# Kernel optimization log

Hardware: AMD Instinct MI355X
Metric: run time of the kernel (lower is better)

The kernel has to match this reference:

```python
import jax, jax.numpy as jnp
import numpy as np

B, H, L, D, LBL = 512, 64, 528, 32, 10
NI = 64          # number of interval breakpoints
W = 128          # vf MLP width
N_STEPS = 256    # fixed Tsit5 steps over [t0, t1]

# Tsit5 Butcher tableau
C2, C3, C4, C5, C6 = 0.161, 0.327, 0.9, 0.9800255409045097, 1.0
A21 = 0.161
A31, A32 = -0.008480655492356989, 0.335480655492357
A41, A42, A43 = 2.8971530571054935, -6.359448489975075, 4.3622954328695815
A51, A52, A53, A54 = 5.325864828439257, -11.748883564062828, 7.4955393428898365, -0.09249506636175525
A61, A62, A63, A64, A65 = 5.86145544294642, -12.92096931784711, 8.159367898576159, -0.071584973281401, -0.028269050394068383
B1, B2, B3, B4, B5, B6 = 0.09646076681806523, 0.01, 0.4798896504144996, 1.379008574103742, -3.290069515436081, 2.324710524099774


def _linear_init(k, out_dim, in_dim):
    lim = 1.0 / np.sqrt(in_dim)
    kw, kb = jax.random.split(k)
    w = jax.random.uniform(kw, (out_dim, in_dim), jnp.float32, -lim, lim)
    b = jax.random.uniform(kb, (out_dim,), jnp.float32, -lim, lim)
    return w, b


def setup_inputs() -> dict:
    key = jax.random.key(0)
    ks = jax.random.split(key, 8)
    ts = jnp.linspace(0.0, 1.0, 129, dtype=jnp.float32)
    logsig = 0.1 * jax.random.normal(ks[0], (B, NI + 1, L + 1), jnp.float32)
    x0 = jax.random.normal(ks[1], (B, D), jnp.float32)
    intervals = jnp.linspace(0.0, 1.0, NI, dtype=jnp.float32)
    vf_w0, vf_b0 = _linear_init(ks[2], W, H)
    vf_w1, vf_b1 = _linear_init(ks[3], W, W)
    vf_w2, vf_b2 = _linear_init(ks[4], W, W)
    vf_w3, vf_b3 = _linear_init(ks[5], H * L, W)
    l1_w, l1_b = _linear_init(ks[6], H, D)
    l2_w, l2_b = _linear_init(ks[7], LBL, H)
    return dict(ts=ts, logsig=logsig, x0=x0, intervals=intervals,
                vf_w0=vf_w0, vf_b0=vf_b0, vf_w1=vf_w1, vf_b1=vf_b1,
                vf_w2=vf_w2, vf_b2=vf_b2, vf_w3=vf_w3, vf_b3=vf_b3,
                l1_w=l1_w, l1_b=l1_b, l2_w=l2_w, l2_b=l2_b)


def reference(ts, logsig, x0, intervals,
              vf_w0, vf_b0, vf_w1, vf_b1, vf_w2, vf_b2, vf_w3, vf_b3,
              l1_w, l1_b, l2_w, l2_b):
    Bn = x0.shape[0]
    Hn = l1_w.shape[0]
    Ln = vf_b3.shape[0] // Hn

    def vf(y):  # y: (B, H) -> (B, H, L)
        h = jax.nn.silu(y @ vf_w0.T + vf_b0)
        h = jax.nn.silu(h @ vf_w1.T + vf_b1)
        h = jax.nn.silu(h @ vf_w2.T + vf_b2)
        out = jnp.tanh(h @ vf_w3.T + vf_b3)
        return out.reshape(Bn, Hn, Ln)

    def func(t, y):
        idx = jnp.searchsorted(intervals, t)
        sig = logsig[:, idx, 1:]          # (B, L)
        return jnp.einsum('bhl,bl->bh', vf(y), sig)

    t0, t1 = ts[0], ts[-1]
    dt = (t1 - t0) / N_STEPS

    def step(y, i):
        t = t0 + i * dt
        k1 = func(t, y)
        k2 = func(t + C2 * dt, y + dt * (A21 * k1))
        k3 = func(t + C3 * dt, y + dt * (A31 * k1 + A32 * k2))
        k4 = func(t + C4 * dt, y + dt * (A41 * k1 + A42 * k2 + A43 * k3))
        k5 = func(t + C5 * dt, y + dt * (A51 * k1 + A52 * k2 + A53 * k3 + A54 * k4))
        k6 = func(t + C6 * dt, y + dt * (A61 * k1 + A62 * k2 + A63 * k3 + A64 * k4 + A65 * k5))
        y_new = y + dt * (B1 * k1 + B2 * k2 + B3 * k3 + B4 * k4 + B5 * k5 + B6 * k6)
        return y_new, None

    y0 = x0 @ l1_w.T + l1_b
    yT, _ = jax.lax.scan(step, y0, jnp.arange(N_STEPS, dtype=jnp.float32))
    return jax.nn.softmax(yT @ l2_w.T + l2_b, axis=-1)
```

## Files before the change

kernel.cpp:

```cpp
#include <hip/hip_runtime.h>
#include <stdint.h>

#define NBLK 256
#define NTHR 512

typedef __attribute__((ext_vector_type(8))) short short8;
typedef __attribute__((ext_vector_type(4))) float float4_;

#define WS_BAR  0
#define WS_HDNF 16384
#define WS_KF   (16384 + 131072)

#define LOADC(p)    __hip_atomic_load((p),  __ATOMIC_RELAXED, __HIP_MEMORY_SCOPE_SYSTEM)
#define STOREC(p,v) __hip_atomic_store((p), (v), __ATOMIC_RELAXED, __HIP_MEMORY_SCOPE_SYSTEM)

__device__ __forceinline__ unsigned short f2bf(float x) {
  union { float f; unsigned u; } v; v.f = x;
  return (unsigned short)((v.u + 0x7fffu + ((v.u >> 16) & 1u)) >> 16);
}
__device__ __forceinline__ float fast_exp(float x) {
  return __builtin_amdgcn_exp2f(x * 1.4426950408889634f);
}
__device__ __forceinline__ float fast_tanh(float x) {
  float e = __builtin_amdgcn_exp2f(x * 2.8853900817779268f);
  return fmaf(-2.0f, __builtin_amdgcn_rcpf(e + 1.0f), 1.0f);
}
__device__ __forceinline__ float fast_silu(float x) {
  float e = fast_exp(-x);
  return x * __builtin_amdgcn_rcpf(1.0f + e);
}

__device__ __forceinline__ void rgbar(unsigned* bar, int h, int Rg, unsigned bn) {
  __syncthreads();
  if (threadIdx.x == 0) {
    unsigned* base = bar + 32 * (32 + Rg * 16);
    unsigned* leaf = base + 32 * (h & 7);
    unsigned* root = base + 32 * 8;
    unsigned* gen  = base + 32 * 9;
    unsigned a = __hip_atomic_fetch_add(leaf, 1u, __ATOMIC_RELAXED, __HIP_MEMORY_SCOPE_SYSTEM);
    if (a == 8u * bn - 1u) {
      unsigned r = __hip_atomic_fetch_add(root, 1u, __ATOMIC_RELAXED, __HIP_MEMORY_SCOPE_SYSTEM);
      if (r == 8u * bn - 1u) STOREC(gen, bn);
    }
    while (LOADC(gen) < bn) __builtin_amdgcn_s_sleep(1);
  }
  __syncthreads();
}

template<int SIN>
__device__ __forceinline__ void rk_stage(
    int stepi, int sg, int h, int Rg, int R, int r0,
    float (&kh)[6], float& y, float t0v, float dtv,
    const float4_ (&wr1)[16], const float4_ (&wr2)[16],
    float b0r, float b1r, float b2r,
    unsigned char* ws, unsigned* BAR, unsigned& rseq,
    const float* logsig, const float* w0,
    unsigned short* w3lds, float* b3lds, float* intv,
    float (*yst)[64], float (*hb1)[128], float (*hb2)[128],
    unsigned short (*hdnS)[128], int* sidxp) {
  const int tid = threadIdx.x;
  const int lane = tid & 63, wv = tid >> 6;
  const int col = lane & 15, qd = lane >> 4;
  const int mrow = tid >> 8, mj = ((tid >> 6) & 3) * 32 + (tid & 31), mhalf = (tid >> 5) & 1;
  unsigned* HDNF = (unsigned*)(ws + WS_HDNF);
  float* KF  = (float*)(ws + WS_KF);

  if (sg > 0 && tid < 128) {
    const float* KFr = KF + ((sg & 1) ^ 1) * 32768;
    constexpr int pi = (SIN == 0) ? 5 : SIN - 1;
    kh[pi] = LOADC(&KFr[(size_t)(r0 + (tid >> 6)) * 64 + (tid & 63)]);
  }
  if (tid < 128) {
    float ystv;
    if constexpr (SIN == 0) {
      if (sg > 0) {
        y += dtv * (0.09646076681806523f * kh[0] + 0.01f * kh[1]
                  + 0.4798896504144996f * kh[2] + 1.379008574103742f * kh[3]
                  - 3.290069515436081f * kh[4] + 2.324710524099774f * kh[5]);
      }
      ystv = y;
    } else if constexpr (SIN == 1) {
      ystv = y + dtv * (0.161f * kh[0]);
    } else if constexpr (SIN == 2) {
      ystv = y + dtv * (-0.008480655492356989f * kh[0] + 0.335480655492357f * kh[1]);
    } else if constexpr (SIN == 3) {
      ystv = y + dtv * (2.8971530571054935f * kh[0] - 6.359448489975075f * kh[1]
                      + 4.3622954328695815f * kh[2]);
    } else if constexpr (SIN == 4) {
      ystv = y + dtv * (5.325864828439257f * kh[0] - 11.748883564062828f * kh[1]
                      + 7.4955393428898365f * kh[2] - 0.09249506636175525f * kh[3]);
    } else {
      ystv = y + dtv * (5.86145544294642f * kh[0] - 12.92096931784711f * kh[1]
                      + 8.159367898576159f * kh[2] - 0.071584973281401f * kh[3]
                      - 0.028269050394068383f * kh[4]);
    }
    yst[tid >> 6][tid & 63] = ystv;
  }
  {
    float tb = __fadd_rn(t0v, __fmul_rn((float)stepi, dtv));
    float t_cur;
    if constexpr (SIN == 0) t_cur = tb;
    else {
      constexpr float cS = (SIN == 1) ? 0.161f : (SIN == 2) ? 0.327f : (SIN == 3) ? 0.9f
                         : (SIN == 4) ? 0.9800255409045097f : 1.0f;
      t_cur = __fadd_rn(tb, __fmul_rn(cS, dtv));
    }
    if (tid < 64) {
      unsigned long long m1 = __ballot(intv[tid] < t_cur);
      if (tid == 0) *sidxp = (int)__popcll(m1);
    }
  }
  __syncthreads();
  const int idx = *sidxp;

  {
    const float4_* wrp = (const float4_*)(w0 + (size_t)mj * 64 + mhalf * 32);
    const float* yp = &yst[mrow][mhalf * 32];
    float ac0 = 0.0f, ac1 = 0.0f;
    #pragma unroll
    for (int i4 = 0; i4 < 8; ++i4) {
      float4_ wvv = wrp[i4];
      float s = fmaf(yp[4*i4+0], wvv[0], yp[4*i4+1] * wvv[1]);
      s = fmaf(yp[4*i4+2], wvv[2], s);
      s = fmaf(yp[4*i4+3], wvv[3], s);
      if (i4 & 1) ac1 += s; else ac0 += s;
    }
    float v = ac0 + ac1;
    v += __shfl_xor(v, 32);
    if (mhalf == 0) hb1[mrow][mj] = fast_silu(v + b0r);
  }
  __syncthreads();
  {
    const float* hp = &hb1[mrow][mhalf * 64];
    float ac0 = 0.0f, ac1 = 0.0f;
    #pragma unroll
    for (int i4 = 0; i4 < 16; ++i4) {
      float4_ wvv = wr1[i4];
      float s = fmaf(hp[4*i4+0], wvv[0], hp[4*i4+1] * wvv[1]);
      s = fmaf(hp[4*i4+2], wvv[2], s);
      s = fmaf(hp[4*i4+3], wvv[3], s);
      if (i4 & 1) ac1 += s; else ac0 += s;
    }
    float v = ac0 + ac1;
    v += __shfl_xor(v, 32);
    if (mhalf == 0) hb2[mrow][mj] = fast_silu(v + b1r);
  }
  __syncthreads();
  {
    const float* hp = &hb2[mrow][mhalf * 64];
    float ac0 = 0.0f, ac1 = 0.0f;
    #pragma unroll
    for (int i4 = 0; i4 < 16; ++i4) {
      float4_ wvv = wr2[i4];
      float s = fmaf(hp[4*i4+0], wvv[0], hp[4*i4+1] * wvv[1]);
      s = fmaf(hp[4*i4+2], wvv[2], s);
      s = fmaf(hp[4*i4+3], wvv[3], s);
      if (i4 & 1) ac1 += s; else ac0 += s;
    }
    float v = ac0 + ac1;
    v += __shfl_xor(v, 32);
    if (mhalf == 0) hdnS[mrow][mj] = f2bf(fast_silu(v + b2r));
  }
  __syncthreads();
  if (tid < 128) {
    const int row = tid >> 6, u = tid & 63;
    const int lb = 2 * h + row;
    const int tile = lb >> 4, colp = lb & 15;
    const int j0 = 2 * u;
    const int kb = j0 >> 5, qdp = (j0 >> 3) & 3, jj = j0 & 7;
    unsigned v = (unsigned)hdnS[row][j0] | ((unsigned)hdnS[row][j0 + 1] << 16);
    unsigned i16 = (unsigned)((Rg * 32 + tile * 4 + kb) * 512 + qdp * 128 + colp * 8 + jj);
    STOREC(&HDNF[i16 >> 1], v);
  }
  ++rseq; rgbar(BAR, h, Rg, rseq);

  {
    const unsigned long long* H64 = (const unsigned long long*)HDNF;
    union { unsigned long long u[2]; short8 s; } af[4];
    #pragma unroll
    for (int kb = 0; kb < 4; ++kb) {
      const unsigned i16 = (unsigned)((Rg * 32 + wv * 4 + kb) * 512 + lane * 8);
      af[kb].u[0] = LOADC(&H64[i16 >> 2]);
      af[kb].u[1] = LOADC(&H64[(i16 >> 2) + 1]);
    }
    const float* sp0 = logsig + (size_t)(R + wv * 16 + qd * 4) * 34385 + (size_t)idx * 529 + 1;
    const float* sp1 = sp0 + 34385;
    const float* sp2 = sp0 + 2 * 34385;
    const float* sp3 = sp0 + 3 * 34385;
    float kp[4] = {0.0f, 0.0f, 0.0f, 0.0f};
    #pragma unroll 2
    for (int nt = 0; nt < 33; ++nt) {
      const int l = nt * 16 + col;
      const float bv = b3lds[l];
      float4_ acc; acc[0] = bv; acc[1] = bv; acc[2] = bv; acc[3] = bv;
      #pragma unroll
      for (int kb = 0; kb < 4; ++kb) {
        const short8 bf = *(const short8*)(w3lds + ((nt * 4 + kb) * 64 + lane) * 8);
        acc = __builtin_amdgcn_mfma_f32_16x16x32_bf16(af[kb].s, bf, acc, 0, 0, 0);
      }
      kp[0] = fmaf(fast_tanh(acc[0]), sp0[l], kp[0]);
      kp[1] = fmaf(fast_tanh(acc[1]), sp1[l], kp[1]);
      kp[2] = fmaf(fast_tanh(acc[2]), sp2[l], kp[2]);
      kp[3] = fmaf(fast_tanh(acc[3]), sp3[l], kp[3]);
    }
    #pragma unroll
    for (int r = 0; r < 4; ++r) {
      float v = kp[r];
      v += __shfl_xor(v, 1); v += __shfl_xor(v, 2);
      v += __shfl_xor(v, 4); v += __shfl_xor(v, 8);
      kp[r] = v;
    }
    if (col == 0) {
      float* KFw = KF + (sg & 1) * 32768;
      #pragma unroll
      for (int r = 0; r < 4; ++r)
        STOREC(&KFw[(size_t)(R + wv * 16 + qd * 4 + r) * 64 + h], kp[r]);
    }
  }
  ++rseq; rgbar(BAR, h, Rg, rseq);
}

__global__ void __launch_bounds__(NTHR, 2)
rde_kernel(const float* __restrict__ ts, const float* __restrict__ logsig,
           const float* __restrict__ x0, const float* __restrict__ intervals,
           const float* __restrict__ w0, const float* __restrict__ b0,
           const float* __restrict__ w1, const float* __restrict__ b1,
           const float* __restrict__ w2, const float* __restrict__ b2,
           const float* __restrict__ w3, const float* __restrict__ b3,
           const float* __restrict__ l1w, const float* __restrict__ l1b,
           const float* __restrict__ l2w, const float* __restrict__ l2b,
           float* out, unsigned char* ws) {
  const int tid = threadIdx.x;
  const int g = blockIdx.x;
  const int Rg = (g >> 1) & 3;
  const int h  = ((g >> 3) << 1) | (g & 1);
  const int R = Rg * 128;
  const int r0 = R + 2 * h;
  unsigned* BAR = (unsigned*)(ws + WS_BAR);
  unsigned rseq = 0;

  __shared__ __attribute__((aligned(16))) unsigned short w3lds[67584];
  __shared__ float b3lds[528];
  __shared__ float intv[64];
  __shared__ float yst[2][64];
  __shared__ float hb1[2][128];
  __shared__ float hb2[2][128];
  __shared__ __attribute__((aligned(8))) unsigned short hdnS[2][128];
  __shared__ int sidx;

  if (tid < 64) intv[tid] = intervals[tid];
  for (int e = tid; e < 528; e += NTHR) b3lds[e] = b3[(size_t)h * 528 + e];

  for (int e = tid; e < 8448; e += NTHR) {
    const int ln = e & 63, kb = (e >> 6) & 3, nt = e >> 8;
    const float* src = w3 + ((size_t)(h * 528 + nt * 16 + (ln & 15))) * 128 + kb * 32 + (ln >> 4) * 8;
    union { unsigned short s[8]; short8 v; } p;
    #pragma unroll
    for (int j = 0; j < 8; ++j) p.s[j] = f2bf(src[j]);
    *(short8*)(w3lds + e * 8) = p.v;
  }

  const int mj = ((tid >> 6) & 3) * 32 + (tid & 31), mhalf = (tid >> 5) & 1;
  float4_ wr1[16], wr2[16];
  {
    const float4_* s1 = (const float4_*)(w1 + (size_t)mj * 128 + mhalf * 64);
    const float4_* s2 = (const float4_*)(w2 + (size_t)mj * 128 + mhalf * 64);
    #pragma unroll
    for (int i = 0; i < 16; ++i) { wr1[i] = s1[i]; wr2[i] = s2[i]; }
  }
  const float b0r = b0[mj], b1r = b1[mj], b2r = b2[mj];

  float y = 0.0f, kh[6];
  #pragma unroll
  for (int i = 0; i < 6; ++i) kh[i] = 0.0f;
  if (tid < 128) {
    const int row = tid >> 6, hh = tid & 63;
    float acc = l1b[hh];
    const float4_* xr = (const float4_*)(x0 + (size_t)(r0 + row) * 32);
    const float4_* wr = (const float4_*)(l1w + (size_t)hh * 32);
    #pragma unroll
    for (int d = 0; d < 8; ++d) {
      float4_ xv = xr[d], wvv = wr[d];
      acc = fmaf(xv[0], wvv[0], acc); acc = fmaf(xv[1], wvv[1], acc);
      acc = fmaf(xv[2], wvv[2], acc); acc = fmaf(xv[3], wvv[3], acc);
    }
    y = acc;
  }
  const float t0v = ts[0];
  const float dtv = (ts[128] - t0v) * (1.0f / 256.0f);
  __syncthreads();

  for (int stepi = 0; stepi < 256; ++stepi) {
    const int sg = stepi * 6;
    rk_stage<0>(stepi, sg + 0, h, Rg, R, r0, kh, y, t0v, dtv, wr1, wr2, b0r, b1r, b2r,
                ws, BAR, rseq, logsig, w0, w3lds, b3lds, intv, yst, hb1, hb2, hdnS, &sidx);
    rk_stage<1>(stepi, sg + 1, h, Rg, R, r0, kh, y, t0v, dtv, wr1, wr2, b0r, b1r, b2r,
                ws, BAR, rseq, logsig, w0, w3lds, b3lds, intv, yst, hb1, hb2, hdnS, &sidx);
    rk_stage<2>(stepi, sg + 2, h, Rg, R, r0, kh, y, t0v, dtv, wr1, wr2, b0r, b1r, b2r,
                ws, BAR, rseq, logsig, w0, w3lds, b3lds, intv, yst, hb1, hb2, hdnS, &sidx);
    rk_stage<3>(stepi, sg + 3, h, Rg, R, r0, kh, y, t0v, dtv, wr1, wr2, b0r, b1r, b2r,
                ws, BAR, rseq, logsig, w0, w3lds, b3lds, intv, yst, hb1, hb2, hdnS, &sidx);
    rk_stage<4>(stepi, sg + 4, h, Rg, R, r0, kh, y, t0v, dtv, wr1, wr2, b0r, b1r, b2r,
                ws, BAR, rseq, logsig, w0, w3lds, b3lds, intv, yst, hb1, hb2, hdnS, &sidx);
    rk_stage<5>(stepi, sg + 5, h, Rg, R, r0, kh, y, t0v, dtv, wr1, wr2, b0r, b1r, b2r,
                ws, BAR, rseq, logsig, w0, w3lds, b3lds, intv, yst, hb1, hb2, hdnS, &sidx);
  }

  {
    float* KF = (float*)(ws + WS_KF);
    if (tid < 128) {
      const int row = tid >> 6, hh = tid & 63;
      kh[5] = LOADC(&KF[(size_t)32768 + (size_t)(r0 + row) * 64 + hh]);
      y += dtv * (0.09646076681806523f * kh[0] + 0.01f * kh[1]
                + 0.4798896504144996f * kh[2] + 1.379008574103742f * kh[3]
                - 3.290069515436081f * kh[4] + 2.324710524099774f * kh[5]);
      yst[row][hh] = y;
    }
    __syncthreads();
    if (tid < 20) {
      const int row = tid / 10, c = tid % 10;
      float acc = l2b[c];
      const float* wr = l2w + c * 64;
      #pragma unroll
      for (int i2 = 0; i2 < 64; ++i2) acc = fmaf(yst[row][i2], wr[i2], acc);
      hb1[row][c] = acc;
    }
    __syncthreads();
    if (tid < 2) {
      const int row = tid;
      float mx = -1e30f;
      for (int c = 0; c < 10; ++c) mx = fmaxf(mx, hb1[row][c]);
      float ev[10], den = 0.0f;
      for (int c = 0; c < 10; ++c) { ev[c] = expf(hb1[row][c] - mx); den += ev[c]; }
      const float rd = 1.0f / den;
      for (int c = 0; c < 10; ++c) out[(size_t)(r0 + row) * 10 + c] = ev[c] * rd;
    }
  }
}

extern "C" void kernel_launch(void* const* d_in, const int* in_sizes, int n_in,
                              void* d_out, int out_size, void* d_ws, size_t ws_size,
                              hipStream_t stream) {
  (void)in_sizes; (void)n_in; (void)out_size; (void)ws_size;
  const float* ts        = (const float*)d_in[0];
  const float* logsig    = (const float*)d_in[1];
  const float* x0        = (const float*)d_in[2];
  const float* intervals = (const float*)d_in[3];
  const float* w0        = (const float*)d_in[4];
  const float* b0        = (const float*)d_in[5];
  const float* w1        = (const float*)d_in[6];
  const float* b1        = (const float*)d_in[7];
  const float* w2        = (const float*)d_in[8];
  const float* b2        = (const float*)d_in[9];
  const float* w3        = (const float*)d_in[10];
  const float* b3        = (const float*)d_in[11];
  const float* l1w       = (const float*)d_in[12];
  const float* l1b       = (const float*)d_in[13];
  const float* l2w       = (const float*)d_in[14];
  const float* l2b       = (const float*)d_in[15];
  float* out = (float*)d_out;
  unsigned char* ws = (unsigned char*)d_ws;

  hipMemsetAsync(d_ws, 0, 12288, stream);

  void* args[] = { &ts, &logsig, &x0, &intervals, &w0, &b0, &w1, &b1,
                   &w2, &b2, &w3, &b3, &l1w, &l1b, &l2w, &l2b, &out, &ws };
  hipLaunchCooperativeKernel((void*)rde_kernel, dim3(NBLK), dim3(NTHR), args, 0, stream);
}
```

Before: 42.98 ms.

## Compute hidden MLP redundantly per block with MFMA, removing one grid barrier per stage

Each block now computes the three hidden MLP layers for all 128 rows of its group with bf16 MFMA, using weights pre-packed into the workspace. The y state is published through global memory instead of the hidden activations, so each RK stage needs one group barrier instead of two. The RK state update also moves into the MFMA output layout. The cost is redundant hidden-layer compute in every block, bf16 precision in the hidden layers (y is split into hi/lo bf16 parts for the first layer), and launch bounds lowered to one block per SIMD set.

```diff
diff --git a/kernel.cpp b/kernel.cpp
--- a/kernel.cpp
+++ b/kernel.cpp
@@ -8,8 +8,10 @@
 typedef __attribute__((ext_vector_type(4))) float float4_;
 
 #define WS_BAR  0
-#define WS_HDNF 16384
-#define WS_KF   (16384 + 131072)
+#define WS_YST  16384
+#define WS_W0F  (16384 + 262144)
+#define WS_W1F  (WS_W0F + 16384)
+#define WS_W2F  (WS_W1F + 32768)
 
 #define LOADC(p)    __hip_atomic_load((p),  __ATOMIC_RELAXED, __HIP_MEMORY_SCOPE_SYSTEM)
 #define STOREC(p,v) __hip_atomic_store((p), (v), __ATOMIC_RELAXED, __HIP_MEMORY_SCOPE_SYSTEM)
@@ -17,6 +19,9 @@
 __device__ __forceinline__ unsigned short f2bf(float x) {
   union { float f; unsigned u; } v; v.f = x;
   return (unsigned short)((v.u + 0x7fffu + ((v.u >> 16) & 1u)) >> 16);
+}
+__device__ __forceinline__ float bf2f(unsigned short s) {
+  union { unsigned u; float f; } v; v.u = ((unsigned)s) << 16; return v.f;
 }
 __device__ __forceinline__ float fast_exp(float x) {
   return __builtin_amdgcn_exp2f(x * 1.4426950408889634f);
@@ -47,55 +52,60 @@
   __syncthreads();
 }
 
+template<int SINN>
+__device__ __forceinline__ void rk_publish(float (&yv)[4], const float (&khv)[6][4],
+                                           float dtv, int col, int mrow0, int h,
+                                           float* YW) {
+  float ystv[4];
+  #pragma unroll
+  for (int r = 0; r < 4; ++r) {
+    if constexpr (SINN == 0) {
+      yv[r] += dtv * (0.09646076681806523f * khv[0][r] + 0.01f * khv[1][r]
+                    + 0.4798896504144996f * khv[2][r] + 1.379008574103742f * khv[3][r]
+                    - 3.290069515436081f * khv[4][r] + 2.324710524099774f * khv[5][r]);
+      ystv[r] = yv[r];
+    } else if constexpr (SINN == 1) {
+      ystv[r] = yv[r] + dtv * (0.161f * khv[0][r]);
+    } else if constexpr (SINN == 2) {
+      ystv[r] = yv[r] + dtv * (-0.008480655492356989f * khv[0][r]
+                             + 0.335480655492357f * khv[1][r]);
+    } else if constexpr (SINN == 3) {
+      ystv[r] = yv[r] + dtv * (2.8971530571054935f * khv[0][r]
+                             - 6.359448489975075f * khv[1][r]
+                             + 4.3622954328695815f * khv[2][r]);
+    } else if constexpr (SINN == 4) {
+      ystv[r] = yv[r] + dtv * (5.325864828439257f * khv[0][r]
+                             - 11.748883564062828f * khv[1][r]
+                             + 7.4955393428898365f * khv[2][r]
+                             - 0.09249506636175525f * khv[3][r]);
+    } else {
+      ystv[r] = yv[r] + dtv * (5.86145544294642f * khv[0][r]
+                             - 12.92096931784711f * khv[1][r]
+                             + 8.159367898576159f * khv[2][r]
+                             - 0.071584973281401f * khv[3][r]
+                             - 0.028269050394068383f * khv[4][r]);
+    }
+  }
+  if (col == 0) {
+    #pragma unroll
+    for (int r = 0; r < 4; ++r)
+      STOREC(&YW[(size_t)(mrow0 + r) * 64 + h], ystv[r]);
+  }
+}
+
 template<int SIN>
 __device__ __forceinline__ void rk_stage(
-    int stepi, int sg, int h, int Rg, int R, int r0,
-    float (&kh)[6], float& y, float t0v, float dtv,
-    const float4_ (&wr1)[16], const float4_ (&wr2)[16],
-    float b0r, float b1r, float b2r,
+    int stepi, int sg, int h, int Rg, int R,
+    float (&yv)[4], float (&khv)[6][4], float t0v, float dtv,
     unsigned char* ws, unsigned* BAR, unsigned& rseq,
-    const float* logsig, const float* w0,
+    const float* logsig, const float* b0, const float* b1, const float* b2,
     unsigned short* w3lds, float* b3lds, float* intv,
-    float (*yst)[64], float (*hb1)[128], float (*hb2)[128],
-    unsigned short (*hdnS)[128], int* sidxp) {
+    unsigned short* bounce, int* sidxp) {
   const int tid = threadIdx.x;
   const int lane = tid & 63, wv = tid >> 6;
   const int col = lane & 15, qd = lane >> 4;
-  const int mrow = tid >> 8, mj = ((tid >> 6) & 3) * 32 + (tid & 31), mhalf = (tid >> 5) & 1;
-  unsigned* HDNF = (unsigned*)(ws + WS_HDNF);
-  float* KF  = (float*)(ws + WS_KF);
-
-  if (sg > 0 && tid < 128) {
-    const float* KFr = KF + ((sg & 1) ^ 1) * 32768;
-    constexpr int pi = (SIN == 0) ? 5 : SIN - 1;
-    kh[pi] = LOADC(&KFr[(size_t)(r0 + (tid >> 6)) * 64 + (tid & 63)]);
-  }
-  if (tid < 128) {
-    float ystv;
-    if constexpr (SIN == 0) {
-      if (sg > 0) {
-        y += dtv * (0.09646076681806523f * kh[0] + 0.01f * kh[1]
-                  + 0.4798896504144996f * kh[2] + 1.379008574103742f * kh[3]
-                  - 3.290069515436081f * kh[4] + 2.324710524099774f * kh[5]);
-      }
-      ystv = y;
-    } else if constexpr (SIN == 1) {
-      ystv = y + dtv * (0.161f * kh[0]);
-    } else if constexpr (SIN == 2) {
-      ystv = y + dtv * (-0.008480655492356989f * kh[0] + 0.335480655492357f * kh[1]);
-    } else if constexpr (SIN == 3) {
-      ystv = y + dtv * (2.8971530571054935f * kh[0] - 6.359448489975075f * kh[1]
-                      + 4.3622954328695815f * kh[2]);
-    } else if constexpr (SIN == 4) {
-      ystv = y + dtv * (5.325864828439257f * kh[0] - 11.748883564062828f * kh[1]
-                      + 7.4955393428898365f * kh[2] - 0.09249506636175525f * kh[3]);
-    } else {
-      ystv = y + dtv * (5.86145544294642f * kh[0] - 12.92096931784711f * kh[1]
-                      + 8.159367898576159f * kh[2] - 0.071584973281401f * kh[3]
-                      - 0.028269050394068383f * kh[4]);
-    }
-    yst[tid >> 6][tid & 63] = ystv;
-  }
+  const int mrow0 = R + wv * 16 + qd * 4;
+
   {
     float tb = __fadd_rn(t0v, __fmul_rn((float)stepi, dtv));
     float t_cur;
@@ -113,81 +123,99 @@
   __syncthreads();
   const int idx = *sidxp;
 
-  {
-    const float4_* wrp = (const float4_*)(w0 + (size_t)mj * 64 + mhalf * 32);
-    const float* yp = &yst[mrow][mhalf * 32];
-    float ac0 = 0.0f, ac1 = 0.0f;
-    #pragma unroll
-    for (int i4 = 0; i4 < 8; ++i4) {
-      float4_ wvv = wrp[i4];
-      float s = fmaf(yp[4*i4+0], wvv[0], yp[4*i4+1] * wvv[1]);
-      s = fmaf(yp[4*i4+2], wvv[2], s);
-      s = fmaf(yp[4*i4+3], wvv[3], s);
-      if (i4 & 1) ac1 += s; else ac0 += s;
-    }
-    float v = ac0 + ac1;
-    v += __shfl_xor(v, 32);
-    if (mhalf == 0) hb1[mrow][mj] = fast_silu(v + b0r);
-  }
-  __syncthreads();
-  {
-    const float* hp = &hb1[mrow][mhalf * 64];
-    float ac0 = 0.0f, ac1 = 0.0f;
-    #pragma unroll
-    for (int i4 = 0; i4 < 16; ++i4) {
-      float4_ wvv = wr1[i4];
-      float s = fmaf(hp[4*i4+0], wvv[0], hp[4*i4+1] * wvv[1]);
-      s = fmaf(hp[4*i4+2], wvv[2], s);
-      s = fmaf(hp[4*i4+3], wvv[3], s);
-      if (i4 & 1) ac1 += s; else ac0 += s;
-    }
-    float v = ac0 + ac1;
-    v += __shfl_xor(v, 32);
-    if (mhalf == 0) hb2[mrow][mj] = fast_silu(v + b1r);
-  }
-  __syncthreads();
-  {
-    const float* hp = &hb2[mrow][mhalf * 64];
-    float ac0 = 0.0f, ac1 = 0.0f;
-    #pragma unroll
-    for (int i4 = 0; i4 < 16; ++i4) {
-      float4_ wvv = wr2[i4];
-      float s = fmaf(hp[4*i4+0], wvv[0], hp[4*i4+1] * wvv[1]);
-      s = fmaf(hp[4*i4+2], wvv[2], s);
-      s = fmaf(hp[4*i4+3], wvv[3], s);
-      if (i4 & 1) ac1 += s; else ac0 += s;
-    }
-    float v = ac0 + ac1;
-    v += __shfl_xor(v, 32);
-    if (mhalf == 0) hdnS[mrow][mj] = f2bf(fast_silu(v + b2r));
-  }
-  __syncthreads();
-  if (tid < 128) {
-    const int row = tid >> 6, u = tid & 63;
-    const int lb = 2 * h + row;
-    const int tile = lb >> 4, colp = lb & 15;
-    const int j0 = 2 * u;
-    const int kb = j0 >> 5, qdp = (j0 >> 3) & 3, jj = j0 & 7;
-    unsigned v = (unsigned)hdnS[row][j0] | ((unsigned)hdnS[row][j0 + 1] << 16);
-    unsigned i16 = (unsigned)((Rg * 32 + tile * 4 + kb) * 512 + qdp * 128 + colp * 8 + jj);
-    STOREC(&HDNF[i16 >> 1], v);
-  }
-  ++rseq; rgbar(BAR, h, Rg, rseq);
-
-  {
-    const unsigned long long* H64 = (const unsigned long long*)HDNF;
-    union { unsigned long long u[2]; short8 s; } af[4];
-    #pragma unroll
-    for (int kb = 0; kb < 4; ++kb) {
-      const unsigned i16 = (unsigned)((Rg * 32 + wv * 4 + kb) * 512 + lane * 8);
-      af[kb].u[0] = LOADC(&H64[i16 >> 2]);
-      af[kb].u[1] = LOADC(&H64[(i16 >> 2) + 1]);
-    }
-    const float* sp0 = logsig + (size_t)(R + wv * 16 + qd * 4) * 34385 + (size_t)idx * 529 + 1;
+  short8 af[4];
+  {
+    const float* YR = (const float*)(ws + WS_YST) + (size_t)(sg & 1) * 32768;
+    const short8* W0F = (const short8*)(ws + WS_W0F);
+    const short8* W1F = (const short8*)(ws + WS_W1F);
+    const short8* W2F = (const short8*)(ws + WS_W2F);
+    unsigned short* M = bounce + wv * 512;
+
+    short8 a1hi[2], a1lo[2];
+    #pragma unroll
+    for (int kb = 0; kb < 2; ++kb) {
+      union { unsigned long long u[4]; float f[8]; } yr;
+      const unsigned long long* ya = (const unsigned long long*)
+          (YR + (size_t)(R + wv * 16 + (lane & 15)) * 64 + kb * 32 + qd * 8);
+      #pragma unroll
+      for (int j = 0; j < 4; ++j) yr.u[j] = LOADC(ya + j);
+      union { unsigned short s[8]; short8 v; } hi, lo;
+      #pragma unroll
+      for (int j = 0; j < 8; ++j) {
+        unsigned short hb = f2bf(yr.f[j]);
+        hi.s[j] = hb;
+        lo.s[j] = f2bf(yr.f[j] - bf2f(hb));
+      }
+      a1hi[kb] = hi.v; a1lo[kb] = lo.v;
+    }
+
+    short8 a2[4];
+    #pragma unroll
+    for (int kp2 = 0; kp2 < 4; ++kp2) {
+      #pragma unroll
+      for (int th = 0; th < 2; ++th) {
+        const int t = kp2 * 2 + th;
+        float4_ c; c[0] = 0.0f; c[1] = 0.0f; c[2] = 0.0f; c[3] = 0.0f;
+        #pragma unroll
+        for (int kb = 0; kb < 2; ++kb) {
+          const short8 bf = W0F[(t * 2 + kb) * 64 + lane];
+          c = __builtin_amdgcn_mfma_f32_16x16x32_bf16(a1hi[kb], bf, c, 0, 0, 0);
+          c = __builtin_amdgcn_mfma_f32_16x16x32_bf16(a1lo[kb], bf, c, 0, 0, 0);
+        }
+        const float bv = b0[t * 16 + col];
+        #pragma unroll
+        for (int r = 0; r < 4; ++r)
+          M[(qd * 4 + r) * 32 + th * 16 + col] = f2bf(fast_silu(c[r] + bv));
+      }
+      a2[kp2] = *(const short8*)&M[(lane & 15) * 32 + qd * 8];
+    }
+
+    short8 a3[4];
+    #pragma unroll
+    for (int kp2 = 0; kp2 < 4; ++kp2) {
+      #pragma unroll
+      for (int th = 0; th < 2; ++th) {
+        const int t = kp2 * 2 + th;
+        float4_ c; c[0] = 0.0f; c[1] = 0.0f; c[2] = 0.0f; c[3] = 0.0f;
+        #pragma unroll
+        for (int kb = 0; kb < 4; ++kb) {
+          const short8 bf = W1F[(t * 4 + kb) * 64 + lane];
+          c = __builtin_amdgcn_mfma_f32_16x16x32_bf16(a2[kb], bf, c, 0, 0, 0);
+        }
+        const float bv = b1[t * 16 + col];
+        #pragma unroll
+        for (int r = 0; r < 4; ++r)
+          M[(qd * 4 + r) * 32 + th * 16 + col] = f2bf(fast_silu(c[r] + bv));
+      }
+      a3[kp2] = *(const short8*)&M[(lane & 15) * 32 + qd * 8];
+    }
+
+    #pragma unroll
+    for (int kp2 = 0; kp2 < 4; ++kp2) {
+      #pragma unroll
+      for (int th = 0; th < 2; ++th) {
+        const int t = kp2 * 2 + th;
+        float4_ c; c[0] = 0.0f; c[1] = 0.0f; c[2] = 0.0f; c[3] = 0.0f;
+        #pragma unroll
+        for (int kb = 0; kb < 4; ++kb) {
+          const short8 bf = W2F[(t * 4 + kb) * 64 + lane];
+          c = __builtin_amdgcn_mfma_f32_16x16x32_bf16(a3[kb], bf, c, 0, 0, 0);
+        }
+        const float bv = b2[t * 16 + col];
+        #pragma unroll
+        for (int r = 0; r < 4; ++r)
+          M[(qd * 4 + r) * 32 + th * 16 + col] = f2bf(fast_silu(c[r] + bv));
+      }
+      af[kp2] = *(const short8*)&M[(lane & 15) * 32 + qd * 8];
+    }
+  }
+
+  float kp[4] = {0.0f, 0.0f, 0.0f, 0.0f};
+  {
+    const float* sp0 = logsig + (size_t)mrow0 * 34385 + (size_t)idx * 529 + 1;
     const float* sp1 = sp0 + 34385;
     const float* sp2 = sp0 + 2 * 34385;
     const float* sp3 = sp0 + 3 * 34385;
-    float kp[4] = {0.0f, 0.0f, 0.0f, 0.0f};
     #pragma unroll 2
     for (int nt = 0; nt < 33; ++nt) {
       const int l = nt * 16 + col;
@@ -196,7 +224,7 @@
       #pragma unroll
       for (int kb = 0; kb < 4; ++kb) {
         const short8 bf = *(const short8*)(w3lds + ((nt * 4 + kb) * 64 + lane) * 8);
-        acc = __builtin_amdgcn_mfma_f32_16x16x32_bf16(af[kb].s, bf, acc, 0, 0, 0);
+        acc = __builtin_amdgcn_mfma_f32_16x16x32_bf16(af[kb], bf, acc, 0, 0, 0);
       }
       kp[0] = fmaf(fast_tanh(acc[0]), sp0[l], kp[0]);
       kp[1] = fmaf(fast_tanh(acc[1]), sp1[l], kp[1]);
@@ -210,17 +238,20 @@
       v += __shfl_xor(v, 4); v += __shfl_xor(v, 8);
       kp[r] = v;
     }
-    if (col == 0) {
-      float* KFw = KF + (sg & 1) * 32768;
-      #pragma unroll
-      for (int r = 0; r < 4; ++r)
-        STOREC(&KFw[(size_t)(R + wv * 16 + qd * 4 + r) * 64 + h], kp[r]);
-    }
-  }
+  }
+
+  #pragma unroll
+  for (int r = 0; r < 4; ++r) khv[SIN][r] = kp[r];
+  {
+    float* YW = (float*)(ws + WS_YST) + (size_t)((sg + 1) & 1) * 32768;
+    constexpr int SINN = (SIN == 5) ? 0 : SIN + 1;
+    rk_publish<SINN>(yv, khv, dtv, col, mrow0, h, YW);
+  }
+
   ++rseq; rgbar(BAR, h, Rg, rseq);
 }
 
-__global__ void __launch_bounds__(NTHR, 2)
+__global__ void __launch_bounds__(NTHR, 1)
 rde_kernel(const float* __restrict__ ts, const float* __restrict__ logsig,
            const float* __restrict__ x0, const float* __restrict__ intervals,
            const float* __restrict__ w0, const float* __restrict__ b0,
@@ -234,18 +265,20 @@
   const int g = blockIdx.x;
   const int Rg = (g >> 1) & 3;
   const int h  = ((g >> 3) << 1) | (g & 1);
-  const int R = Rg * 128;
+  const int R  = Rg * 128;
   const int r0 = R + 2 * h;
+  const int lane = tid & 63, wv = tid >> 6;
+  const int col = lane & 15, qd = lane >> 4;
+  const int mrow0 = R + wv * 16 + qd * 4;
   unsigned* BAR = (unsigned*)(ws + WS_BAR);
   unsigned rseq = 0;
 
   __shared__ __attribute__((aligned(16))) unsigned short w3lds[67584];
+  __shared__ __attribute__((aligned(16))) unsigned short bounce[8 * 512];
   __shared__ float b3lds[528];
   __shared__ float intv[64];
-  __shared__ float yst[2][64];
-  __shared__ float hb1[2][128];
-  __shared__ float hb2[2][128];
-  __shared__ __attribute__((aligned(8))) unsigned short hdnS[2][128];
+  __shared__ float yfin[2][64];
+  __shared__ float hcls[2][10];
   __shared__ int sidx;
 
   if (tid < 64) intv[tid] = intervals[tid];
@@ -260,61 +293,90 @@
     *(short8*)(w3lds + e * 8) = p.v;
   }
 
-  const int mj = ((tid >> 6) & 3) * 32 + (tid & 31), mhalf = (tid >> 5) & 1;
-  float4_ wr1[16], wr2[16];
-  {
-    const float4_* s1 = (const float4_*)(w1 + (size_t)mj * 128 + mhalf * 64);
-    const float4_* s2 = (const float4_*)(w2 + (size_t)mj * 128 + mhalf * 64);
-    #pragma unroll
-    for (int i = 0; i < 16; ++i) { wr1[i] = s1[i]; wr2[i] = s2[i]; }
-  }
-  const float b0r = b0[mj], b1r = b1[mj], b2r = b2[mj];
-
-  float y = 0.0f, kh[6];
+  for (int e = tid; e < 1024; e += NTHR) {
+    const int ln = e & 63, kb = (e >> 6) & 1, t = e >> 7;
+    const float* src = w0 + (size_t)(t * 16 + (ln & 15)) * 64 + kb * 32 + (ln >> 4) * 8;
+    union { unsigned short s[8]; short8 v; } p;
+    #pragma unroll
+    for (int j = 0; j < 8; ++j) p.s[j] = f2bf(src[j]);
+    ((short8*)(ws + WS_W0F))[e] = p.v;
+  }
+  for (int e = tid; e < 2048; e += NTHR) {
+    const int ln = e & 63, kb = (e >> 6) & 3, t = e >> 8;
+    const float* src = w1 + (size_t)(t * 16 + (ln & 15)) * 128 + kb * 32 + (ln >> 4) * 8;
+    union { unsigned short s[8]; short8 v; } p;
+    #pragma unroll
+    for (int j = 0; j < 8; ++j) p.s[j] = f2bf(src[j]);
+    ((short8*)(ws + WS_W1F))[e] = p.v;
+  }
+  for (int e = tid; e < 2048; e += NTHR) {
+    const int ln = e & 63, kb = (e >> 6) & 3, t = e >> 8;
+    const float* src = w2 + (size_t)(t * 16 + (ln & 15)) * 128 + kb * 32 + (ln >> 4) * 8;
+    union { unsigned short s[8]; short8 v; } p;
+    #pragma unroll
+    for (int j = 0; j < 8; ++j) p.s[j] = f2bf(src[j]);
+    ((short8*)(ws + WS_W2F))[e] = p.v;
+  }
+
+  float yv[4], khv[6][4];
   #pragma unroll
-  for (int i = 0; i < 6; ++i) kh[i] = 0.0f;
-  if (tid < 128) {
-    const int row = tid >> 6, hh = tid & 63;
-    float acc = l1b[hh];
-    const float4_* xr = (const float4_*)(x0 + (size_t)(r0 + row) * 32);
-    const float4_* wr = (const float4_*)(l1w + (size_t)hh * 32);
-    #pragma unroll
-    for (int d = 0; d < 8; ++d) {
-      float4_ xv = xr[d], wvv = wr[d];
-      acc = fmaf(xv[0], wvv[0], acc); acc = fmaf(xv[1], wvv[1], acc);
-      acc = fmaf(xv[2], wvv[2], acc); acc = fmaf(xv[3], wvv[3], acc);
-    }
-    y = acc;
+  for (int i = 0; i < 6; ++i)
+    #pragma unroll
+    for (int r = 0; r < 4; ++r) khv[i][r] = 0.0f;
+  {
+    const float4_* wr = (const float4_*)(l1w + (size_t)h * 32);
+    float4_ wv4[8];
+    #pragma unroll
+    for (int d = 0; d < 8; ++d) wv4[d] = wr[d];
+    const float bb = l1b[h];
+    #pragma unroll
+    for (int r = 0; r < 4; ++r) {
+      const float4_* xr = (const float4_*)(x0 + (size_t)(mrow0 + r) * 32);
+      float acc = bb;
+      #pragma unroll
+      for (int d = 0; d < 8; ++d) {
+        float4_ xv = xr[d];
+        acc = fmaf(xv[0], wv4[d][0], acc); acc = fmaf(xv[1], wv4[d][1], acc);
+        acc = fmaf(xv[2], wv4[d][2], acc); acc = fmaf(xv[3], wv4[d][3], acc);
+      }
+      yv[r] = acc;
+    }
   }
   const float t0v = ts[0];
   const float dtv = (ts[128] - t0v) * (1.0f / 256.0f);
   __syncthreads();
 
+  {
+    float* YW = (float*)(ws + WS_YST);
+    if (col == 0) {
+      #pragma unroll
+      for (int r = 0; r < 4; ++r)
+        STOREC(&YW[(size_t)(mrow0 + r) * 64 + h], yv[r]);
+    }
+  }
+  ++rseq; rgbar(BAR, h, Rg, rseq);
+
   for (int stepi = 0; stepi < 256; ++stepi) {
     const int sg = stepi * 6;
-    rk_stage<0>(stepi, sg + 0, h, Rg, R, r0, kh, y, t0v, dtv, wr1, wr2, b0r, b1r, b2r,
-                ws, BAR, rseq, logsig, w0, w3lds, b3lds, intv, yst, hb1, hb2, hdnS, &sidx);
-    rk_stage<1>(stepi, sg + 1, h, Rg, R, r0, kh, y, t0v, dtv, wr1, wr2, b0r, b1r, b2r,
-                ws, BAR, rseq, logsig, w0, w3lds, b3lds, intv, yst, hb1, hb2, hdnS, &sidx);
-    rk_stage<2>(stepi, sg + 2, h, Rg, R, r0, kh, y, t0v, dtv, wr1, wr2, b0r, b1r, b2r,
-                ws, BAR, rseq, logsig, w0, w3lds, b3lds, intv, yst, hb1, hb2, hdnS, &sidx);
-    rk_stage<3>(stepi, sg + 3, h, Rg, R, r0, kh, y, t0v, dtv, wr1, wr2, b0r, b1r, b2r,
-                ws, BAR, rseq, logsig, w0, w3lds, b3lds, intv, yst, hb1, hb2, hdnS, &sidx);
-    rk_stage<4>(stepi, sg + 4, h, Rg, R, r0, kh, y, t0v, dtv, wr1, wr2, b0r, b1r, b2r,
-                ws, BAR, rseq, logsig, w0, w3lds, b3lds, intv, yst, hb1, hb2, hdnS, &sidx);
-    rk_stage<5>(stepi, sg + 5, h, Rg, R, r0, kh, y, t0v, dtv, wr1, wr2, b0r, b1r, b2r,
-                ws, BAR, rseq, logsig, w0, w3lds, b3lds, intv, yst, hb1, hb2, hdnS, &sidx);
-  }
-
-  {
-    float* KF = (float*)(ws + WS_KF);
+    rk_stage<0>(stepi, sg + 0, h, Rg, R, yv, khv, t0v, dtv, ws, BAR, rseq,
+                logsig, b0, b1, b2, w3lds, b3lds, intv, bounce, &sidx);
+    rk_stage<1>(stepi, sg + 1, h, Rg, R, yv, khv, t0v, dtv, ws, BAR, rseq,
+                logsig, b0, b1, b2, w3lds, b3lds, intv, bounce, &sidx);
+    rk_stage<2>(stepi, sg + 2, h, Rg, R, yv, khv, t0v, dtv, ws, BAR, rseq,
+                logsig, b0, b1, b2, w3lds, b3lds, intv, bounce, &sidx);
+    rk_stage<3>(stepi, sg + 3, h, Rg, R, yv, khv, t0v, dtv, ws, BAR, rseq,
+                logsig, b0, b1, b2, w3lds, b3lds, intv, bounce, &sidx);
+    rk_stage<4>(stepi, sg + 4, h, Rg, R, yv, khv, t0v, dtv, ws, BAR, rseq,
+                logsig, b0, b1, b2, w3lds, b3lds, intv, bounce, &sidx);
+    rk_stage<5>(stepi, sg + 5, h, Rg, R, yv, khv, t0v, dtv, ws, BAR, rseq,
+                logsig, b0, b1, b2, w3lds, b3lds, intv, bounce, &sidx);
+  }
+
+  {
+    const float* YF = (const float*)(ws + WS_YST);
     if (tid < 128) {
       const int row = tid >> 6, hh = tid & 63;
-      kh[5] = LOADC(&KF[(size_t)32768 + (size_t)(r0 + row) * 64 + hh]);
-      y += dtv * (0.09646076681806523f * kh[0] + 0.01f * kh[1]
-                + 0.4798896504144996f * kh[2] + 1.379008574103742f * kh[3]
-                - 3.290069515436081f * kh[4] + 2.324710524099774f * kh[5]);
-      yst[row][hh] = y;
+      yfin[row][hh] = LOADC(&YF[(size_t)(r0 + row) * 64 + hh]);
     }
     __syncthreads();
     if (tid < 20) {
@@ -322,16 +384,16 @@
       float acc = l2b[c];
       const float* wr = l2w + c * 64;
       #pragma unroll
-      for (int i2 = 0; i2 < 64; ++i2) acc = fmaf(yst[row][i2], wr[i2], acc);
-      hb1[row][c] = acc;
+      for (int i2 = 0; i2 < 64; ++i2) acc = fmaf(yfin[row][i2], wr[i2], acc);
+      hcls[row][c] = acc;
     }
     __syncthreads();
     if (tid < 2) {
       const int row = tid;
       float mx = -1e30f;
-      for (int c = 0; c < 10; ++c) mx = fmaxf(mx, hb1[row][c]);
+      for (int c = 0; c < 10; ++c) mx = fmaxf(mx, hcls[row][c]);
       float ev[10], den = 0.0f;
-      for (int c = 0; c < 10; ++c) { ev[c] = expf(hb1[row][c] - mx); den += ev[c]; }
+      for (int c = 0; c < 10; ++c) { ev[c] = expf(hcls[row][c] - mx); den += ev[c]; }
       const float rd = 1.0f / den;
       for (int c = 0; c < 10; ++c) out[(size_t)(r0 + row) * 10 + c] = ev[c] * rd;
     }
```

After: 77.61 ms. 1.81x slower.
